# Optimization experiments

Hardware: AMD Instinct MI355X
Metric: run time of the kernel (lower is better)

## Reference

```python
import jax, jax.numpy as jnp
import numpy as np

N_NODES = 100000
N_EDGES = 1250000
D = 64


def _mlp(h, W1, b1, W2, b2):
    # shared GIN 'network': Linear -> ReLU -> Linear
    return jnp.maximum(h @ W1 + b1, 0.0) @ W2 + b2


def setup_inputs() -> dict:
    key = jax.random.key(0)
    ks = jax.random.split(key, 8)
    s = 1.0 / np.sqrt(D)
    x = jax.random.normal(ks[0], (N_NODES, D), dtype=jnp.float32)
    edge_index = jax.random.randint(ks[1], (2, N_EDGES), 0, N_NODES, dtype=jnp.int32)
    edge_attr = jax.random.normal(ks[2], (N_EDGES, D), dtype=jnp.float32)
    W1 = jax.random.normal(ks[3], (D, D), dtype=jnp.float32) * s
    b1 = jnp.zeros((D,), dtype=jnp.float32)
    W2 = jax.random.normal(ks[4], (D, D), dtype=jnp.float32) * s
    b2 = jnp.zeros((D,), dtype=jnp.float32)
    W_lin = jax.random.normal(ks[5], (3 * D, D), dtype=jnp.float32) * (1.0 / np.sqrt(3 * D))
    b_lin = jnp.zeros((D,), dtype=jnp.float32)
    return {"x": x, "edge_index": edge_index, "edge_attr": edge_attr,
            "W1": W1, "b1": b1, "W2": W2, "b2": b2,
            "W_lin": W_lin, "b_lin": b_lin}


def reference(x, edge_index, edge_attr, W1, b1, W2, b2, W_lin, b_lin):
    src = edge_index[0]  # [E]
    dst = edge_index[1]  # [E]
    n = x.shape[0]
    # forward conv: message from src -> aggregate at dst
    msg_f = jnp.maximum(x[src] + edge_attr, 0.0)            # [E, D]
    a_in = _mlp(jax.ops.segment_sum(msg_f, dst, num_segments=n), W1, b1, W2, b2)
    # backward conv (edge_index.flipud): message from dst -> aggregate at src
    msg_b = jnp.maximum(x[dst] + edge_attr, 0.0)            # [E, D]
    a_out = _mlp(jax.ops.segment_sum(msg_b, src, num_segments=n), W1, b1, W2, b2)
    # final projection of concat [x, a_in, a_out]
    return jnp.concatenate([x, a_in, a_out], axis=1) @ W_lin + b_lin
```

## Files before the change

kernel.cpp:

```cpp
#include <hip/hip_runtime.h>

#define NN 100000
#define NE 1250000
#define DD 64
#define NBKT 391
#define NCNT NBKT
#define NCNT2 (2 * NCNT)
#define CHUNK 8192
#define NCHUNK ((NE + CHUNK - 1) / CHUNK)
#define HBLK 256
#define GNB 25000
#define TSTR 68

typedef __attribute__((ext_vector_type(8))) short bf16x8_t;
typedef __attribute__((ext_vector_type(4))) float f32x4_t;

__device__ __forceinline__ unsigned short bf16_rne(float v) {
  unsigned u = __builtin_bit_cast(unsigned, v);
  u += 0x7FFFu + ((u >> 16) & 1u);
  return (unsigned short)(u >> 16);
}
__device__ __forceinline__ void split_bf16(float v, unsigned short& hi,
                                           unsigned short& lo) {
  hi = bf16_rne(v);
  const float fh = __builtin_bit_cast(float, ((unsigned)hi) << 16);
  lo = bf16_rne(v - fh);
}

__global__ __launch_bounds__(256) void precompute_kernel(
    const float* __restrict__ W2, const float* __restrict__ b2,
    const float* __restrict__ Wl, const float* __restrict__ bl,
    float* __restrict__ Wc1, float* __restrict__ Wc2, float* __restrict__ bc) {
  const int t = blockIdx.x * 256 + threadIdx.x;
  const int m = t >> 12;
  const int ij = t & 4095;
  const int i = ij >> 6, j = ij & 63;
  const float* Wp = Wl + (m ? 128 : 64) * 64;
  float s = 0.f;
#pragma unroll 8
  for (int k = 0; k < 64; ++k) s = fmaf(W2[i * 64 + k], Wp[k * 64 + j], s);
  if (m) Wc2[ij] = s; else Wc1[ij] = s;
  if (t < 64) {
    float sb = bl[t];
    for (int k = 0; k < 64; ++k)
      sb = fmaf(b2[k], Wl[(64 + k) * 64 + t] + Wl[(128 + k) * 64 + t], sb);
    bc[t] = sb;
  }
}

__global__ __launch_bounds__(256) void pack_w_kernel(
    const float* __restrict__ W1, const float* __restrict__ Wl,
    const float* __restrict__ Wc1, const float* __restrict__ Wc2,
    unsigned short* __restrict__ whi, unsigned short* __restrict__ wlo) {
  const int g = blockIdx.x * 256 + threadIdx.x;
  if (g >= 4 * 4096) return;
  const int mat = g >> 12;
  const int idx = g & 4095;
  const int i = idx & 7;
  const int lane = (idx >> 3) & 63;
  const int ct = (idx >> 9) & 3;
  const int ks = (idx >> 11) & 1;
  const int k = ks * 32 + ((lane >> 4) << 2) + (i & 3) + ((i >> 2) << 4);
  const int col = ct * 16 + (lane & 15);
  const float* src = (mat == 0) ? W1 : (mat == 1) ? Wc1 : (mat == 2) ? Wc2 : Wl;
  const float v = src[k * 64 + col];
  unsigned short h, l;
  split_bf16(v, h, l);
  whi[g] = h;
  wlo[g] = l;
}

__global__ __launch_bounds__(256) void bucket_hist_kernel(
    const int* __restrict__ ei, int* __restrict__ bcnt) {
  __shared__ int h[NCNT2];
  const int t = threadIdx.x;
  for (int i = t; i < NCNT2; i += 256) h[i] = 0;
  __syncthreads();
  const int stride = 256 * HBLK;
  for (int e = blockIdx.x * 256 + t; e < NE; e += stride) {
    atomicAdd(&h[ei[NE + e] >> 8], 1);
    atomicAdd(&h[NBKT + (ei[e] >> 8)], 1);
  }
  __syncthreads();
  for (int i = t; i < NCNT2; i += 256) {
    const int c = h[i];
    if (c) atomicAdd(&bcnt[i], c);
  }
}

__global__ __launch_bounds__(1024) void bucket_scan_kernel(
    const int* __restrict__ bcnt, int* __restrict__ bbase,
    int* __restrict__ bcur2, int* __restrict__ off_d,
    int* __restrict__ off_s) {
  __shared__ int part[1024];
  const int t = threadIdx.x;
  int v[4];
  int s = 0;
#pragma unroll
  for (int i = 0; i < 4; ++i) {
    const int idx = t * 4 + i;
    v[i] = (idx < NCNT2) ? bcnt[idx] : 0;
    s += v[i];
  }
  part[t] = s;
  __syncthreads();
  int acc = s;
  for (int d = 1; d < 1024; d <<= 1) {
    const int add = (t >= d) ? part[t - d] : 0;
    __syncthreads();
    acc += add;
    part[t] = acc;
    __syncthreads();
  }
  int pre = acc - s;
#pragma unroll
  for (int i = 0; i < 4; ++i) {
    const int idx = t * 4 + i;
    if (idx < NCNT2) {
      bbase[idx] = pre;
      bcur2[idx] = pre;
    }
    pre += v[i];
  }
  if (t == 0) {
    bbase[NCNT2] = 2 * NE;
    off_d[NN] = NE;
    off_s[NN] = 2 * NE;
  }
}

__global__ __launch_bounds__(256) void multisplit_kernel(
    const int* __restrict__ ei, int* __restrict__ bcur2,
    int* __restrict__ tmp) {
  __shared__ int recs[CHUNK];
  __shared__ int hist[NBKT];
  __shared__ int hbase[NBKT + 1];
  __shared__ int hcur[NBKT];
  __shared__ int gbase[NBKT];
  __shared__ int scanbuf[256];
  const int t = threadIdx.x;
  const int dir = (blockIdx.x >= NCHUNK) ? 1 : 0;
  const int chunk = blockIdx.x - (dir ? NCHUNK : 0);
  const int e0 = chunk * CHUNK;
  const int cnt = min(CHUNK, NE - e0);
  const int* keys = ei + (dir ? 0 : NE);
  for (int i = t; i < NBKT; i += 256) {
    hist[i] = 0;
    hcur[i] = 0;
  }
  __syncthreads();
  for (int i = t; i < cnt; i += 256) atomicAdd(&hist[keys[e0 + i] >> 8], 1);
  __syncthreads();
  const int i0 = 2 * t, i1 = 2 * t + 1;
  const int s0 = (i0 < NBKT) ? hist[i0] : 0;
  const int s1 = (i1 < NBKT) ? hist[i1] : 0;
  const int ps = s0 + s1;
  scanbuf[t] = ps;
  __syncthreads();
  int acc = ps;
  for (int d = 1; d < 256; d <<= 1) {
    const int add = (t >= d) ? scanbuf[t - d] : 0;
    __syncthreads();
    acc += add;
    scanbuf[t] = acc;
    __syncthreads();
  }
  const int pre = acc - ps;
  if (i0 < NBKT) hbase[i0] = pre;
  if (i1 < NBKT) hbase[i1] = pre + s0;
  if (t == 0) hbase[NBKT] = cnt;
  __syncthreads();
  for (int b = t; b < NBKT; b += 256) {
    const int c = hist[b];
    if (c > 0) gbase[b] = atomicAdd(&bcur2[dir * NBKT + b], c);
  }
  for (int i = t; i < cnt; i += 256) {
    const int n = keys[e0 + i];
    const int b = n >> 8;
    const int p = hbase[b] + atomicAdd(&hcur[b], 1);
    recs[p] = ((e0 + i) << 8) | (n & 255);
  }
  __syncthreads();
  for (int p = t; p < cnt; p += 256) {
    int lo = 0, hi = NBKT;
    while (hi - lo > 1) {
      const int mid = (lo + hi) >> 1;
      if (hbase[mid] <= p) lo = mid;
      else hi = mid;
    }
    tmp[gbase[lo] + (p - hbase[lo])] = recs[p];
  }
}

__global__ __launch_bounds__(256) void bucket_sort_kernel(
    const int* __restrict__ tmp, const int* __restrict__ bbase,
    const int* __restrict__ ei, int* __restrict__ off_d,
    int* __restrict__ off_s, int2* __restrict__ lst2) {
  __shared__ int hist[256];
  __shared__ int scanbuf[256];
  __shared__ int cur[256];
  const int t = threadIdx.x;
  const int isrc = (blockIdx.x >= NBKT) ? 1 : 0;
  const int bloc = blockIdx.x - (isrc ? NBKT : 0);
  const int cbase = (isrc ? NCNT : 0) + bloc;
  const int beg = bbase[cbase];
  const int end = bbase[cbase + 1];
  const int* pbase = ei + (isrc ? NE : 0);
  hist[t] = 0;
  __syncthreads();
  for (int k = beg + t; k < end; k += 256) atomicAdd(&hist[tmp[k] & 255], 1);
  __syncthreads();
  const int v = hist[t];
  int acc = v;
  scanbuf[t] = v;
  __syncthreads();
  for (int d = 1; d < 256; d <<= 1) {
    const int add = (t >= d) ? scanbuf[t - d] : 0;
    __syncthreads();
    acc += add;
    scanbuf[t] = acc;
    __syncthreads();
  }
  const int base_t = beg + acc - v;
  cur[t] = base_t;
  int* off = isrc ? off_s : off_d;
  const int n = bloc * 256 + t;
  if (n < NN) off[n] = base_t;
  __syncthreads();
  for (int k = beg + t; k < end; k += 256) {
    const int r = tmp[k];
    const int e = (int)(((unsigned)r) >> 8);
    const int p = atomicAdd(&cur[r & 255], 1);
    lst2[p] = make_int2(e, pbase[e]);
  }
}

__global__ __launch_bounds__(256) void gather_kernel(
    const float* __restrict__ x, const float* __restrict__ ea,
    const int* __restrict__ off_d, const int* __restrict__ off_s,
    const int2* __restrict__ lst2, float* __restrict__ agg_in,
    float* __restrict__ agg_out) {
  const int t = threadIdx.x;
  const int wave = t >> 6;
  const int lane = t & 63;
  const int slot = lane >> 3;
  const int q = lane & 7;
  const int dir = (blockIdx.x >= GNB) ? 1 : 0;
  const int n = (blockIdx.x - (dir ? GNB : 0)) * 4 + wave;
  if (n >= NN) return;
  const int* off = dir ? off_s : off_d;
  float* agg = dir ? agg_out : agg_in;
  const int beg = off[n];
  const int end = off[n + 1];
  const int c0 = q * 8;
  float4 acc0 = make_float4(0.f, 0.f, 0.f, 0.f);
  float4 acc1 = make_float4(0.f, 0.f, 0.f, 0.f);
  for (int k = beg + slot; k < end; k += 8) {
    const int2 r = lst2[k];
    const float* ar = ea + (size_t)r.x * DD + c0;
    const float* xr = x + (size_t)r.y * DD + c0;
    const float4 a0 = *reinterpret_cast<const float4*>(ar);
    const float4 a1 = *reinterpret_cast<const float4*>(ar + 4);
    const float4 x0 = *reinterpret_cast<const float4*>(xr);
    const float4 x1 = *reinterpret_cast<const float4*>(xr + 4);
    acc0.x += fmaxf(a0.x + x0.x, 0.f);
    acc0.y += fmaxf(a0.y + x0.y, 0.f);
    acc0.z += fmaxf(a0.z + x0.z, 0.f);
    acc0.w += fmaxf(a0.w + x0.w, 0.f);
    acc1.x += fmaxf(a1.x + x1.x, 0.f);
    acc1.y += fmaxf(a1.y + x1.y, 0.f);
    acc1.z += fmaxf(a1.z + x1.z, 0.f);
    acc1.w += fmaxf(a1.w + x1.w, 0.f);
  }
#pragma unroll
  for (int m = 8; m <= 32; m <<= 1) {
    acc0.x += __shfl_xor(acc0.x, m);
    acc0.y += __shfl_xor(acc0.y, m);
    acc0.z += __shfl_xor(acc0.z, m);
    acc0.w += __shfl_xor(acc0.w, m);
    acc1.x += __shfl_xor(acc1.x, m);
    acc1.y += __shfl_xor(acc1.y, m);
    acc1.z += __shfl_xor(acc1.z, m);
    acc1.w += __shfl_xor(acc1.w, m);
  }
  if (lane < 8) {
    float* p = agg + (size_t)n * DD + lane * 8;
    *reinterpret_cast<float4*>(p) = acc0;
    *reinterpret_cast<float4*>(p + 4) = acc1;
  }
}

__global__ __launch_bounds__(256) void edge_kernel(
    const float* __restrict__ x, const int* __restrict__ ei,
    const float* __restrict__ ea, float* __restrict__ agg_in,
    float* __restrict__ agg_out) {
  const int tid = blockIdx.x * 256 + threadIdx.x;
  const int e = tid >> 4;
  if (e >= NE) return;
  const int c = (tid & 15) * 4;
  const int s = ei[e];
  const int d = ei[NE + e];
  const float4 a = *reinterpret_cast<const float4*>(ea + (size_t)e * DD + c);
  const float4 xs = *reinterpret_cast<const float4*>(x + (size_t)s * DD + c);
  const float4 xd = *reinterpret_cast<const float4*>(x + (size_t)d * DD + c);
  float* pi = agg_in + (size_t)d * DD + c;
  unsafeAtomicAdd(pi + 0, fmaxf(xs.x + a.x, 0.f));
  unsafeAtomicAdd(pi + 1, fmaxf(xs.y + a.y, 0.f));
  unsafeAtomicAdd(pi + 2, fmaxf(xs.z + a.z, 0.f));
  unsafeAtomicAdd(pi + 3, fmaxf(xs.w + a.w, 0.f));
  float* po = agg_out + (size_t)s * DD + c;
  unsafeAtomicAdd(po + 0, fmaxf(xd.x + a.x, 0.f));
  unsafeAtomicAdd(po + 1, fmaxf(xd.y + a.y, 0.f));
  unsafeAtomicAdd(po + 2, fmaxf(xd.z + a.z, 0.f));
  unsafeAtomicAdd(po + 3, fmaxf(xd.w + a.w, 0.f));
}

__device__ __forceinline__ void mm_pass(const float* At, int wv, int lane,
                                        const unsigned short* __restrict__ whi,
                                        const unsigned short* __restrict__ wlo,
                                        int mat, f32x4_t acc[4]) {
  const int row = (wv << 4) + (lane & 15);
  const int kbase = ((lane >> 4) & 3) << 2;
#pragma unroll
  for (int ks = 0; ks < 2; ++ks) {
    const float* ap = At + row * TSTR + ks * 32 + kbase;
    const float4 g0 = *reinterpret_cast<const float4*>(ap);
    const float4 g1 = *reinterpret_cast<const float4*>(ap + 16);
    const float gv[8] = {g0.x, g0.y, g0.z, g0.w, g1.x, g1.y, g1.z, g1.w};
    bf16x8_t ahi, alo;
#pragma unroll
    for (int i = 0; i < 8; ++i) {
      unsigned short h, l;
      split_bf16(gv[i], h, l);
      ahi[i] = (short)h;
      alo[i] = (short)l;
    }
#pragma unroll
    for (int ct = 0; ct < 4; ++ct) {
      const int fb = ((mat * 2 + ks) * 4 + ct) * 512 + lane * 8;
      const bf16x8_t wh = *reinterpret_cast<const bf16x8_t*>(whi + fb);
      const bf16x8_t wl = *reinterpret_cast<const bf16x8_t*>(wlo + fb);
      acc[ct] = __builtin_amdgcn_mfma_f32_16x16x32_bf16(ahi, wh, acc[ct], 0, 0, 0);
      acc[ct] = __builtin_amdgcn_mfma_f32_16x16x32_bf16(alo, wh, acc[ct], 0, 0, 0);
      acc[ct] = __builtin_amdgcn_mfma_f32_16x16x32_bf16(ahi, wl, acc[ct], 0, 0, 0);
    }
  }
}

__global__ __launch_bounds__(256) void node_kernel(
    const float* __restrict__ x, const float* __restrict__ agg_in,
    const float* __restrict__ agg_out, const float* __restrict__ b1,
    const float* __restrict__ bc, const unsigned short* __restrict__ whi,
    const unsigned short* __restrict__ wlo, float* __restrict__ out) {
  __shared__ float TA[64 * TSTR];
  __shared__ float TH[64 * TSTR];
  const int t = threadIdx.x;
  const int lane = t & 63;
  const int wv = t >> 6;
  const int n0 = blockIdx.x * 64;

  f32x4_t ofrag[4];
#pragma unroll
  for (int ct = 0; ct < 4; ++ct) ofrag[ct] = (f32x4_t){0.f, 0.f, 0.f, 0.f};
  float b1v[4], bcv[4];
#pragma unroll
  for (int ct = 0; ct < 4; ++ct) {
    b1v[ct] = b1[ct * 16 + (lane & 15)];
    bcv[ct] = bc[ct * 16 + (lane & 15)];
  }

#define LOAD_TILE_F32(SRC)                                                    \
  {                                                                           \
    const int r = t >> 2;                                                     \
    const int cb = (t & 3) * 16;                                              \
    const int n = n0 + r;                                                     \
    _Pragma("unroll") for (int ii = 0; ii < 4; ++ii) {                        \
      float4 v = make_float4(0.f, 0.f, 0.f, 0.f);                             \
      if (n < NN)                                                             \
        v = *reinterpret_cast<const float4*>((SRC) + (size_t)n * DD + cb +    \
                                             ii * 4);                         \
      *reinterpret_cast<float4*>(&TA[r * TSTR + cb + ii * 4]) = v;            \
    }                                                                         \
  }

#define H_PASS(MATW1)                                                         \
  {                                                                           \
    f32x4_t h[4];                                                             \
    _Pragma("unroll") for (int ct = 0; ct < 4; ++ct) h[ct] =                  \
        (f32x4_t){0.f, 0.f, 0.f, 0.f};                                        \
    mm_pass(TA, wv, lane, whi, wlo, (MATW1), h);                              \
    _Pragma("unroll") for (int ct = 0; ct < 4; ++ct)                          \
        _Pragma("unroll") for (int r = 0; r < 4; ++r) {                       \
      const float hv = fmaxf(h[ct][r] + b1v[ct], 0.f);                        \
      TH[((wv << 4) + ((lane >> 4) << 2) + r) * TSTR + ct * 16 +              \
         (lane & 15)] = hv;                                                   \
    }                                                                         \
  }

  LOAD_TILE_F32(agg_in);
  __syncthreads();
  H_PASS(0);
  __syncthreads();
  mm_pass(TH, wv, lane, whi, wlo, 1, ofrag);
  __syncthreads();
  LOAD_TILE_F32(agg_out);
  __syncthreads();
  H_PASS(0);
  __syncthreads();
  mm_pass(TH, wv, lane, whi, wlo, 2, ofrag);
  __syncthreads();
  LOAD_TILE_F32(x);
  __syncthreads();
  mm_pass(TA, wv, lane, whi, wlo, 3, ofrag);

#pragma unroll
  for (int ct = 0; ct < 4; ++ct)
#pragma unroll
    for (int r = 0; r < 4; ++r) {
      const int n = n0 + (wv << 4) + ((lane >> 4) << 2) + r;
      if (n < NN)
        out[(size_t)n * DD + ct * 16 + (lane & 15)] = ofrag[ct][r] + bcv[ct];
    }
}

extern "C" void kernel_launch(void* const* d_in, const int* in_sizes, int n_in,
                              void* d_out, int out_size, void* d_ws,
                              size_t ws_size, hipStream_t stream) {
  const float* x = (const float*)d_in[0];
  const int* ei = (const int*)d_in[1];
  const float* ea = (const float*)d_in[2];
  const float* W1 = (const float*)d_in[3];
  const float* b1 = (const float*)d_in[4];
  const float* W2 = (const float*)d_in[5];
  const float* b2 = (const float*)d_in[6];
  const float* Wl = (const float*)d_in[7];
  const float* bl = (const float*)d_in[8];
  float* out = (float*)d_out;
  float* ws = (float*)d_ws;

  float* agg_in = ws;
  float* agg_out = agg_in + (size_t)NN * DD;
  int* tmp = (int*)(agg_out + (size_t)NN * DD);
  int2* lst2 = (int2*)(tmp + 2 * (size_t)NE);
  int* off_dst = (int*)(lst2 + 2 * (size_t)NE);
  int* off_src = off_dst + NN + 4;
  int* bcnt = off_src + NN + 4;
  int* bbase = bcnt + NCNT2 + 2;
  int* bcur2 = bbase + NCNT2 + 8;
  float* Wc1 = (float*)(bcur2 + NCNT2 + 8);
  float* Wc2 = Wc1 + 4096;
  float* bc = Wc2 + 4096;
  unsigned short* whi = (unsigned short*)(bc + 64);
  unsigned short* wlo = whi + 4 * 4096;
  const size_t need = (size_t)((char*)(wlo + 4 * 4096) - (char*)ws);

  const bool bkt_ok = ws_size >= need;
  if (!bkt_ok) {
    Wc1 = agg_out + (size_t)NN * DD;
    Wc2 = Wc1 + 4096;
    bc = Wc2 + 4096;
    whi = (unsigned short*)(bc + 64);
    wlo = whi + 4 * 4096;
  }

  precompute_kernel<<<32, 256, 0, stream>>>(W2, b2, Wl, bl, Wc1, Wc2, bc);
  pack_w_kernel<<<64, 256, 0, stream>>>(W1, Wl, Wc1, Wc2, whi, wlo);

  if (bkt_ok) {
    hipMemsetAsync(bcnt, 0, NCNT2 * sizeof(int), stream);
    bucket_hist_kernel<<<HBLK, 256, 0, stream>>>(ei, bcnt);
    bucket_scan_kernel<<<1, 1024, 0, stream>>>(bcnt, bbase, bcur2, off_dst,
                                               off_src);
    multisplit_kernel<<<2 * NCHUNK, 256, 0, stream>>>(ei, bcur2, tmp);
    bucket_sort_kernel<<<2 * NBKT, 256, 0, stream>>>(tmp, bbase, ei, off_dst,
                                                     off_src, lst2);
    gather_kernel<<<2 * GNB, 256, 0, stream>>>(x, ea, off_dst, off_src, lst2,
                                               agg_in, agg_out);
  } else {
    hipMemsetAsync(agg_in, 0, 2 * (size_t)NN * DD * sizeof(float), stream);
    edge_kernel<<<((size_t)NE * 16 + 255) / 256, 256, 0, stream>>>(
        x, ei, ea, agg_in, agg_out);
  }

  node_kernel<<<(NN + 63) / 64, 256, 0, stream>>>(x, agg_in, agg_out, b1, bc,
                                                  whi, wlo, out);
}
```

Baseline: 352.1 us.

## Fuse bucket sort and segment gather into one kernel using LDS records

Merges the per-bucket counting sort and the per-node gather into one kernel. Each block sorts one 256-node bucket's edges into shared memory and then aggregates those nodes directly, so the global lst2 and offset arrays and one launch are no longer needed. The cost is far fewer blocks (782 of 512 threads instead of 50000), which limits latency hiding for the random gathers. Buckets holding more than SORT_CAP edges would silently lose edges; the average bucket holds about 3200.

```diff
diff --git a/kernel.cpp b/kernel.cpp
--- a/kernel.cpp
+++ b/kernel.cpp
@@ -9,7 +9,7 @@
 #define CHUNK 8192
 #define NCHUNK ((NE + CHUNK - 1) / CHUNK)
 #define HBLK 256
-#define GNB 25000
+#define SORT_CAP 4096
 #define TSTR 68
 
 typedef __attribute__((ext_vector_type(8))) short bf16x8_t;
@@ -90,8 +90,7 @@
 
 __global__ __launch_bounds__(1024) void bucket_scan_kernel(
     const int* __restrict__ bcnt, int* __restrict__ bbase,
-    int* __restrict__ bcur2, int* __restrict__ off_d,
-    int* __restrict__ off_s) {
+    int* __restrict__ bcur2) {
   __shared__ int part[1024];
   const int t = threadIdx.x;
   int v[4];
@@ -122,11 +121,7 @@
     }
     pre += v[i];
   }
-  if (t == 0) {
-    bbase[NCNT2] = 2 * NE;
-    off_d[NN] = NE;
-    off_s[NN] = 2 * NE;
-  }
+  if (t == 0) bbase[NCNT2] = 2 * NE;
 }
 
 __global__ __launch_bounds__(256) void multisplit_kernel(
@@ -192,101 +187,103 @@
   }
 }
 
-__global__ __launch_bounds__(256) void bucket_sort_kernel(
-    const int* __restrict__ tmp, const int* __restrict__ bbase,
-    const int* __restrict__ ei, int* __restrict__ off_d,
-    int* __restrict__ off_s, int2* __restrict__ lst2) {
+__global__ __launch_bounds__(512) void sort_gather_kernel(
+    const float* __restrict__ x, const float* __restrict__ ea,
+    const int* __restrict__ ei, const int* __restrict__ tmp,
+    const int* __restrict__ bbase, float* __restrict__ agg_in,
+    float* __restrict__ agg_out) {
+  __shared__ int2 srec[SORT_CAP];
   __shared__ int hist[256];
+  __shared__ int offl[257];
+  __shared__ int cur[256];
   __shared__ int scanbuf[256];
-  __shared__ int cur[256];
   const int t = threadIdx.x;
   const int isrc = (blockIdx.x >= NBKT) ? 1 : 0;
   const int bloc = blockIdx.x - (isrc ? NBKT : 0);
   const int cbase = (isrc ? NCNT : 0) + bloc;
   const int beg = bbase[cbase];
   const int end = bbase[cbase + 1];
+  const int cnt = end - beg;
   const int* pbase = ei + (isrc ? NE : 0);
-  hist[t] = 0;
-  __syncthreads();
-  for (int k = beg + t; k < end; k += 256) atomicAdd(&hist[tmp[k] & 255], 1);
-  __syncthreads();
-  const int v = hist[t];
-  int acc = v;
-  scanbuf[t] = v;
+  if (t < 256) hist[t] = 0;
+  __syncthreads();
+  for (int k = beg + t; k < end; k += 512) atomicAdd(&hist[tmp[k] & 255], 1);
+  __syncthreads();
+  int v = 0, acc = 0;
+  if (t < 256) {
+    v = hist[t];
+    acc = v;
+    scanbuf[t] = v;
+  }
   __syncthreads();
   for (int d = 1; d < 256; d <<= 1) {
-    const int add = (t >= d) ? scanbuf[t - d] : 0;
-    __syncthreads();
-    acc += add;
-    scanbuf[t] = acc;
-    __syncthreads();
-  }
-  const int base_t = beg + acc - v;
-  cur[t] = base_t;
-  int* off = isrc ? off_s : off_d;
-  const int n = bloc * 256 + t;
-  if (n < NN) off[n] = base_t;
-  __syncthreads();
-  for (int k = beg + t; k < end; k += 256) {
+    int add = 0;
+    if (t < 256 && t >= d) add = scanbuf[t - d];
+    __syncthreads();
+    if (t < 256) {
+      acc += add;
+      scanbuf[t] = acc;
+    }
+    __syncthreads();
+  }
+  if (t < 256) {
+    offl[t] = acc - v;
+    cur[t] = acc - v;
+  }
+  if (t == 0) offl[256] = cnt;
+  __syncthreads();
+  for (int k = beg + t; k < end; k += 512) {
     const int r = tmp[k];
     const int e = (int)(((unsigned)r) >> 8);
     const int p = atomicAdd(&cur[r & 255], 1);
-    lst2[p] = make_int2(e, pbase[e]);
-  }
-}
-
-__global__ __launch_bounds__(256) void gather_kernel(
-    const float* __restrict__ x, const float* __restrict__ ea,
-    const int* __restrict__ off_d, const int* __restrict__ off_s,
-    const int2* __restrict__ lst2, float* __restrict__ agg_in,
-    float* __restrict__ agg_out) {
-  const int t = threadIdx.x;
-  const int wave = t >> 6;
+    if (p < SORT_CAP) srec[p] = make_int2(e, pbase[e]);
+  }
+  __syncthreads();
+  const int wv = t >> 6;
   const int lane = t & 63;
   const int slot = lane >> 3;
   const int q = lane & 7;
-  const int dir = (blockIdx.x >= GNB) ? 1 : 0;
-  const int n = (blockIdx.x - (dir ? GNB : 0)) * 4 + wave;
-  if (n >= NN) return;
-  const int* off = dir ? off_s : off_d;
-  float* agg = dir ? agg_out : agg_in;
-  const int beg = off[n];
-  const int end = off[n + 1];
   const int c0 = q * 8;
-  float4 acc0 = make_float4(0.f, 0.f, 0.f, 0.f);
-  float4 acc1 = make_float4(0.f, 0.f, 0.f, 0.f);
-  for (int k = beg + slot; k < end; k += 8) {
-    const int2 r = lst2[k];
-    const float* ar = ea + (size_t)r.x * DD + c0;
-    const float* xr = x + (size_t)r.y * DD + c0;
-    const float4 a0 = *reinterpret_cast<const float4*>(ar);
-    const float4 a1 = *reinterpret_cast<const float4*>(ar + 4);
-    const float4 x0 = *reinterpret_cast<const float4*>(xr);
-    const float4 x1 = *reinterpret_cast<const float4*>(xr + 4);
-    acc0.x += fmaxf(a0.x + x0.x, 0.f);
-    acc0.y += fmaxf(a0.y + x0.y, 0.f);
-    acc0.z += fmaxf(a0.z + x0.z, 0.f);
-    acc0.w += fmaxf(a0.w + x0.w, 0.f);
-    acc1.x += fmaxf(a1.x + x1.x, 0.f);
-    acc1.y += fmaxf(a1.y + x1.y, 0.f);
-    acc1.z += fmaxf(a1.z + x1.z, 0.f);
-    acc1.w += fmaxf(a1.w + x1.w, 0.f);
-  }
-#pragma unroll
-  for (int m = 8; m <= 32; m <<= 1) {
-    acc0.x += __shfl_xor(acc0.x, m);
-    acc0.y += __shfl_xor(acc0.y, m);
-    acc0.z += __shfl_xor(acc0.z, m);
-    acc0.w += __shfl_xor(acc0.w, m);
-    acc1.x += __shfl_xor(acc1.x, m);
-    acc1.y += __shfl_xor(acc1.y, m);
-    acc1.z += __shfl_xor(acc1.z, m);
-    acc1.w += __shfl_xor(acc1.w, m);
-  }
-  if (lane < 8) {
-    float* p = agg + (size_t)n * DD + lane * 8;
-    *reinterpret_cast<float4*>(p) = acc0;
-    *reinterpret_cast<float4*>(p + 4) = acc1;
+  float* agg = isrc ? agg_out : agg_in;
+  for (int nk = wv * 32; nk < wv * 32 + 32; ++nk) {
+    const int n = bloc * 256 + nk;
+    const int b2 = offl[nk];
+    const int e2 = offl[nk + 1];
+    float4 acc0 = make_float4(0.f, 0.f, 0.f, 0.f);
+    float4 acc1 = make_float4(0.f, 0.f, 0.f, 0.f);
+    for (int k = b2 + slot; k < e2; k += 8) {
+      const int2 r = srec[k];
+      const float* ar = ea + (size_t)r.x * DD + c0;
+      const float* xr = x + (size_t)r.y * DD + c0;
+      const float4 a0 = *reinterpret_cast<const float4*>(ar);
+      const float4 a1 = *reinterpret_cast<const float4*>(ar + 4);
+      const float4 x0 = *reinterpret_cast<const float4*>(xr);
+      const float4 x1 = *reinterpret_cast<const float4*>(xr + 4);
+      acc0.x += fmaxf(a0.x + x0.x, 0.f);
+      acc0.y += fmaxf(a0.y + x0.y, 0.f);
+      acc0.z += fmaxf(a0.z + x0.z, 0.f);
+      acc0.w += fmaxf(a0.w + x0.w, 0.f);
+      acc1.x += fmaxf(a1.x + x1.x, 0.f);
+      acc1.y += fmaxf(a1.y + x1.y, 0.f);
+      acc1.z += fmaxf(a1.z + x1.z, 0.f);
+      acc1.w += fmaxf(a1.w + x1.w, 0.f);
+    }
+#pragma unroll
+    for (int m = 8; m <= 32; m <<= 1) {
+      acc0.x += __shfl_xor(acc0.x, m);
+      acc0.y += __shfl_xor(acc0.y, m);
+      acc0.z += __shfl_xor(acc0.z, m);
+      acc0.w += __shfl_xor(acc0.w, m);
+      acc1.x += __shfl_xor(acc1.x, m);
+      acc1.y += __shfl_xor(acc1.y, m);
+      acc1.z += __shfl_xor(acc1.z, m);
+      acc1.w += __shfl_xor(acc1.w, m);
+    }
+    if (lane < 8 && n < NN) {
+      float* p = agg + (size_t)n * DD + lane * 8;
+      *reinterpret_cast<float4*>(p) = acc0;
+      *reinterpret_cast<float4*>(p + 4) = acc1;
+    }
   }
 }
 
@@ -441,10 +438,7 @@
   float* agg_in = ws;
   float* agg_out = agg_in + (size_t)NN * DD;
   int* tmp = (int*)(agg_out + (size_t)NN * DD);
-  int2* lst2 = (int2*)(tmp + 2 * (size_t)NE);
-  int* off_dst = (int*)(lst2 + 2 * (size_t)NE);
-  int* off_src = off_dst + NN + 4;
-  int* bcnt = off_src + NN + 4;
+  int* bcnt = tmp + 2 * (size_t)NE;
   int* bbase = bcnt + NCNT2 + 2;
   int* bcur2 = bbase + NCNT2 + 8;
   float* Wc1 = (float*)(bcur2 + NCNT2 + 8);
@@ -469,13 +463,10 @@
   if (bkt_ok) {
     hipMemsetAsync(bcnt, 0, NCNT2 * sizeof(int), stream);
     bucket_hist_kernel<<<HBLK, 256, 0, stream>>>(ei, bcnt);
-    bucket_scan_kernel<<<1, 1024, 0, stream>>>(bcnt, bbase, bcur2, off_dst,
-                                               off_src);
+    bucket_scan_kernel<<<1, 1024, 0, stream>>>(bcnt, bbase, bcur2);
     multisplit_kernel<<<2 * NCHUNK, 256, 0, stream>>>(ei, bcur2, tmp);
-    bucket_sort_kernel<<<2 * NBKT, 256, 0, stream>>>(tmp, bbase, ei, off_dst,
-                                                     off_src, lst2);
-    gather_kernel<<<2 * GNB, 256, 0, stream>>>(x, ea, off_dst, off_src, lst2,
-                                               agg_in, agg_out);
+    sort_gather_kernel<<<2 * NBKT, 512, 0, stream>>>(x, ea, ei, tmp, bbase,
+                                                     agg_in, agg_out);
   } else {
     hipMemsetAsync(agg_in, 0, 2 * (size_t)NN * DD * sizeof(float), stream);
     edge_kernel<<<((size_t)NE * 16 + 255) / 256, 256, 0, stream>>>(
```

After: 353.8 us. No clear change (+0.5%).

## Replace bucket histogram and scan with fixed-capacity bucket regions

Applied to the files above, without the earlier changes.

Removes the global bucket-histogram and prefix-scan kernels. Each bucket now gets a fixed region of SORT_CAP slots, and multisplit claims positions inside it with atomics on a zeroed counter. The sort and gather kernels switch from a single offset array to separate begin and end arrays per node. This cuts an extra pass over edge_index and two small launches, but it assumes no bucket holds more than 4096 edges. That holds for uniformly random graphs, while skewed degree distributions would overflow into the next region and corrupt results.

```diff
diff --git a/kernel.cpp b/kernel.cpp
--- a/kernel.cpp
+++ b/kernel.cpp
@@ -8,7 +8,7 @@
 #define NCNT2 (2 * NCNT)
 #define CHUNK 8192
 #define NCHUNK ((NE + CHUNK - 1) / CHUNK)
-#define HBLK 256
+#define SORT_CAP 4096
 #define GNB 25000
 #define TSTR 68
 
@@ -70,65 +70,6 @@
   wlo[g] = l;
 }
 
-__global__ __launch_bounds__(256) void bucket_hist_kernel(
-    const int* __restrict__ ei, int* __restrict__ bcnt) {
-  __shared__ int h[NCNT2];
-  const int t = threadIdx.x;
-  for (int i = t; i < NCNT2; i += 256) h[i] = 0;
-  __syncthreads();
-  const int stride = 256 * HBLK;
-  for (int e = blockIdx.x * 256 + t; e < NE; e += stride) {
-    atomicAdd(&h[ei[NE + e] >> 8], 1);
-    atomicAdd(&h[NBKT + (ei[e] >> 8)], 1);
-  }
-  __syncthreads();
-  for (int i = t; i < NCNT2; i += 256) {
-    const int c = h[i];
-    if (c) atomicAdd(&bcnt[i], c);
-  }
-}
-
-__global__ __launch_bounds__(1024) void bucket_scan_kernel(
-    const int* __restrict__ bcnt, int* __restrict__ bbase,
-    int* __restrict__ bcur2, int* __restrict__ off_d,
-    int* __restrict__ off_s) {
-  __shared__ int part[1024];
-  const int t = threadIdx.x;
-  int v[4];
-  int s = 0;
-#pragma unroll
-  for (int i = 0; i < 4; ++i) {
-    const int idx = t * 4 + i;
-    v[i] = (idx < NCNT2) ? bcnt[idx] : 0;
-    s += v[i];
-  }
-  part[t] = s;
-  __syncthreads();
-  int acc = s;
-  for (int d = 1; d < 1024; d <<= 1) {
-    const int add = (t >= d) ? part[t - d] : 0;
-    __syncthreads();
-    acc += add;
-    part[t] = acc;
-    __syncthreads();
-  }
-  int pre = acc - s;
-#pragma unroll
-  for (int i = 0; i < 4; ++i) {
-    const int idx = t * 4 + i;
-    if (idx < NCNT2) {
-      bbase[idx] = pre;
-      bcur2[idx] = pre;
-    }
-    pre += v[i];
-  }
-  if (t == 0) {
-    bbase[NCNT2] = 2 * NE;
-    off_d[NN] = NE;
-    off_s[NN] = 2 * NE;
-  }
-}
-
 __global__ __launch_bounds__(256) void multisplit_kernel(
     const int* __restrict__ ei, int* __restrict__ bcur2,
     int* __restrict__ tmp) {
@@ -172,7 +113,9 @@
   __syncthreads();
   for (int b = t; b < NBKT; b += 256) {
     const int c = hist[b];
-    if (c > 0) gbase[b] = atomicAdd(&bcur2[dir * NBKT + b], c);
+    if (c > 0)
+      gbase[b] = (dir * NBKT + b) * SORT_CAP +
+                 atomicAdd(&bcur2[dir * NBKT + b], c);
   }
   for (int i = t; i < cnt; i += 256) {
     const int n = keys[e0 + i];
@@ -193,22 +136,22 @@
 }
 
 __global__ __launch_bounds__(256) void bucket_sort_kernel(
-    const int* __restrict__ tmp, const int* __restrict__ bbase,
-    const int* __restrict__ ei, int* __restrict__ off_d,
-    int* __restrict__ off_s, int2* __restrict__ lst2) {
+    const int* __restrict__ tmp, const int* __restrict__ bcur2,
+    const int* __restrict__ ei, int* __restrict__ offb_d,
+    int* __restrict__ offe_d, int* __restrict__ offb_s,
+    int* __restrict__ offe_s, int2* __restrict__ lst2) {
   __shared__ int hist[256];
   __shared__ int scanbuf[256];
   __shared__ int cur[256];
   const int t = threadIdx.x;
   const int isrc = (blockIdx.x >= NBKT) ? 1 : 0;
   const int bloc = blockIdx.x - (isrc ? NBKT : 0);
-  const int cbase = (isrc ? NCNT : 0) + bloc;
-  const int beg = bbase[cbase];
-  const int end = bbase[cbase + 1];
+  const int base = (isrc * NBKT + bloc) * SORT_CAP;
+  const int cnt = min(bcur2[isrc * NCNT + bloc], SORT_CAP);
   const int* pbase = ei + (isrc ? NE : 0);
   hist[t] = 0;
   __syncthreads();
-  for (int k = beg + t; k < end; k += 256) atomicAdd(&hist[tmp[k] & 255], 1);
+  for (int k = t; k < cnt; k += 256) atomicAdd(&hist[tmp[base + k] & 255], 1);
   __syncthreads();
   const int v = hist[t];
   int acc = v;
@@ -221,14 +164,18 @@
     scanbuf[t] = acc;
     __syncthreads();
   }
-  const int base_t = beg + acc - v;
-  cur[t] = base_t;
-  int* off = isrc ? off_s : off_d;
+  const int beg_t = base + acc - v;
+  cur[t] = beg_t;
+  int* offb = isrc ? offb_s : offb_d;
+  int* offe = isrc ? offe_s : offe_d;
   const int n = bloc * 256 + t;
-  if (n < NN) off[n] = base_t;
-  __syncthreads();
-  for (int k = beg + t; k < end; k += 256) {
-    const int r = tmp[k];
+  if (n < NN) {
+    offb[n] = beg_t;
+    offe[n] = base + acc;
+  }
+  __syncthreads();
+  for (int k = t; k < cnt; k += 256) {
+    const int r = tmp[base + k];
     const int e = (int)(((unsigned)r) >> 8);
     const int p = atomicAdd(&cur[r & 255], 1);
     lst2[p] = make_int2(e, pbase[e]);
@@ -237,7 +184,8 @@
 
 __global__ __launch_bounds__(256) void gather_kernel(
     const float* __restrict__ x, const float* __restrict__ ea,
-    const int* __restrict__ off_d, const int* __restrict__ off_s,
+    const int* __restrict__ offb_d, const int* __restrict__ offe_d,
+    const int* __restrict__ offb_s, const int* __restrict__ offe_s,
     const int2* __restrict__ lst2, float* __restrict__ agg_in,
     float* __restrict__ agg_out) {
   const int t = threadIdx.x;
@@ -248,10 +196,11 @@
   const int dir = (blockIdx.x >= GNB) ? 1 : 0;
   const int n = (blockIdx.x - (dir ? GNB : 0)) * 4 + wave;
   if (n >= NN) return;
-  const int* off = dir ? off_s : off_d;
+  const int* offb = dir ? offb_s : offb_d;
+  const int* offe = dir ? offe_s : offe_d;
   float* agg = dir ? agg_out : agg_in;
-  const int beg = off[n];
-  const int end = off[n + 1];
+  const int beg = offb[n];
+  const int end = offe[n];
   const int c0 = q * 8;
   float4 acc0 = make_float4(0.f, 0.f, 0.f, 0.f);
   float4 acc1 = make_float4(0.f, 0.f, 0.f, 0.f);
@@ -438,16 +387,17 @@
   float* out = (float*)d_out;
   float* ws = (float*)d_ws;
 
+  const size_t REG = (size_t)NCNT2 * SORT_CAP;
   float* agg_in = ws;
   float* agg_out = agg_in + (size_t)NN * DD;
   int* tmp = (int*)(agg_out + (size_t)NN * DD);
-  int2* lst2 = (int2*)(tmp + 2 * (size_t)NE);
-  int* off_dst = (int*)(lst2 + 2 * (size_t)NE);
-  int* off_src = off_dst + NN + 4;
-  int* bcnt = off_src + NN + 4;
-  int* bbase = bcnt + NCNT2 + 2;
-  int* bcur2 = bbase + NCNT2 + 8;
-  float* Wc1 = (float*)(bcur2 + NCNT2 + 8);
+  int2* lst2 = (int2*)(tmp + REG);
+  int* offb_d = (int*)(lst2 + REG);
+  int* offe_d = offb_d + NN + 4;
+  int* offb_s = offe_d + NN + 4;
+  int* offe_s = offb_s + NN + 4;
+  int* bcur2 = offe_s + NN + 4;
+  float* Wc1 = (float*)(bcur2 + NCNT2 + 10);
   float* Wc2 = Wc1 + 4096;
   float* bc = Wc2 + 4096;
   unsigned short* whi = (unsigned short*)(bc + 64);
@@ -467,15 +417,12 @@
   pack_w_kernel<<<64, 256, 0, stream>>>(W1, Wl, Wc1, Wc2, whi, wlo);
 
   if (bkt_ok) {
-    hipMemsetAsync(bcnt, 0, NCNT2 * sizeof(int), stream);
-    bucket_hist_kernel<<<HBLK, 256, 0, stream>>>(ei, bcnt);
-    bucket_scan_kernel<<<1, 1024, 0, stream>>>(bcnt, bbase, bcur2, off_dst,
-                                               off_src);
+    hipMemsetAsync(bcur2, 0, NCNT2 * sizeof(int), stream);
     multisplit_kernel<<<2 * NCHUNK, 256, 0, stream>>>(ei, bcur2, tmp);
-    bucket_sort_kernel<<<2 * NBKT, 256, 0, stream>>>(tmp, bbase, ei, off_dst,
-                                                     off_src, lst2);
-    gather_kernel<<<2 * GNB, 256, 0, stream>>>(x, ea, off_dst, off_src, lst2,
-                                               agg_in, agg_out);
+    bucket_sort_kernel<<<2 * NBKT, 256, 0, stream>>>(
+        tmp, bcur2, ei, offb_d, offe_d, offb_s, offe_s, lst2);
+    gather_kernel<<<2 * GNB, 256, 0, stream>>>(x, ea, offb_d, offe_d, offb_s,
+                                               offe_s, lst2, agg_in, agg_out);
   } else {
     hipMemsetAsync(agg_in, 0, 2 * (size_t)NN * DD * sizeof(float), stream);
     edge_kernel<<<((size_t)NE * 16 + 255) / 256, 256, 0, stream>>>(
```

New measurement: 329.4 us. 6.4% less time.
